# Kernel tuning notes

Hardware: AMD Instinct MI355X
Metric: run time of the kernel (lower is better)

## Reference

```python
import jax, jax.numpy as jnp
import numpy as np

# Static problem dims (match input_specs / init_kwargs)
B, NQ, C, H = 2, 900, 256, 8
HGT, WID = 64, 64            # single-scale feature map (input_spatial_shapes = [[64, 64]])
N = HGT * WID                # 4096 keys
DH = C // H                  # head dim 32
RPE_HID = 512
STRIDE = 16                  # feature_stride


def setup_inputs() -> dict:
    key = jax.random.key(0)
    ks = jax.random.split(key, 24)
    p = lambda k, shape: jax.random.normal(k, shape, jnp.float32) * 0.02
    # reference boxes (cx, cy, w, h) in pixel coords of a 1024x1024 image
    ref = jax.random.uniform(ks[0], (B, NQ, 1, 4), jnp.float32)
    ref = jnp.concatenate([ref[..., :2] * (WID * STRIDE), ref[..., 2:] * 128.0], axis=-1)
    return {
        "vggt_features": jnp.zeros((1,), jnp.float32),  # unused by forward (kept for signature fidelity)
        "query": jax.random.normal(ks[1], (B, NQ, C), jnp.float32),
        "reference_2d": ref,
        "k_input_flatten": jax.random.normal(ks[2], (B, N, C), jnp.float32),
        "v_input_flatten": jax.random.normal(ks[3], (B, N, C), jnp.float32),
        "input_spatial_shapes": jnp.array([[HGT, WID]], jnp.int32),
        "input_padding_mask": jnp.zeros((B, N), jnp.bool_),
        # cpb_mlp1 (x) and cpb_mlp2 (y): Linear(2,512)+ReLU+Linear(512,H,no bias); stored as [in,out]
        "W1x": p(ks[4], (2, RPE_HID)), "b1x": jnp.zeros((RPE_HID,), jnp.float32), "W2x": p(ks[5], (RPE_HID, H)),
        "W1y": p(ks[6], (2, RPE_HID)), "b1y": jnp.zeros((RPE_HID,), jnp.float32), "W2y": p(ks[7], (RPE_HID, H)),
        "Wq": p(ks[8], (C, C)), "bq": jnp.zeros((C,), jnp.float32),
        "Wk": p(ks[9], (C, C)), "bk": jnp.zeros((C,), jnp.float32),
        "Wv": p(ks[10], (C, C)), "bv": jnp.zeros((C,), jnp.float32),
        "Wp": p(ks[11], (C, C)), "bp": jnp.zeros((C,), jnp.float32),
    }


def _mlp(d, W1, b1, W2):
    return jax.nn.relu(d @ W1 + b1) @ W2


def reference(vggt_features, query, reference_2d, k_input_flatten, v_input_flatten,
              input_spatial_shapes, input_padding_mask,
              W1x, b1x, W2x, W1y, b1y, W2y, Wq, bq, Wk, bk, Wv, bv, Wp, bp):
    h, w = HGT, WID  # static (input_spatial_shapes[0] == [HGT, WID])
    scale = DH ** -0.5
    # cxcywh -> xyxy: [B, NQ, 1, 4]
    xyxy = jnp.concatenate([reference_2d[..., :2] - reference_2d[..., 2:] / 2,
                            reference_2d[..., :2] + reference_2d[..., 2:] / 2], axis=-1)
    # pixel-center grid coords (linspace(0.5, w-0.5, w) * stride)
    pos_x = ((jnp.arange(w, dtype=jnp.float32) + 0.5) * STRIDE)[None, None, :, None]
    pos_y = ((jnp.arange(h, dtype=jnp.float32) + 0.5) * STRIDE)[None, None, :, None]
    delta_x = xyxy[..., 0::2] - pos_x  # [B, NQ, w, 2]  (x1, x2 rel. to columns)
    delta_y = xyxy[..., 1::2] - pos_y  # [B, NQ, h, 2]  (y1, y2 rel. to rows)
    rpe_x = _mlp(delta_x, W1x, b1x, W2x)  # [B, NQ, w, H]
    rpe_y = _mlp(delta_y, W1y, b1y, W2y)  # [B, NQ, h, H]
    # broadcast add over (row, col) then flatten spatial -> [B, H, NQ, N]
    rpe = (rpe_x[:, :, None] + rpe_y[:, :, :, None]).reshape(B, NQ, h * w, H).transpose(0, 3, 1, 2)
    q = (query @ Wq + bq).reshape(B, NQ, H, DH).transpose(0, 2, 1, 3) * scale  # [B,H,NQ,DH]
    k = (k_input_flatten @ Wk + bk).reshape(B, N, H, DH).transpose(0, 2, 1, 3)  # [B,H,N,DH]
    v = (v_input_flatten @ Wv + bv).reshape(B, N, H, DH).transpose(0, 2, 1, 3)  # [B,H,N,DH]
    attn = jnp.einsum('bhqd,bhkd->bhqk', q, k) + rpe
    attn = attn + input_padding_mask[:, None, None, :].astype(attn.dtype) * (-100.0)
    # torch.clip_ to finfo(min,max) is an identity on finite values; softmax follows
    attn = jax.nn.softmax(attn, axis=-1)
    x = jnp.einsum('bhqk,bhkd->bhqd', attn, v).transpose(0, 2, 1, 3).reshape(B, NQ, C)
    return x @ Wp + bp
```

## Files before the change

kernel.cpp:

```cpp
#include <hip/hip_runtime.h>
#include <hip/hip_bf16.h>
#include <cmath>

#define B_ 2
#define NQ_ 900
#define N_ 4096
#define LOG2E 1.4426950408889634f

typedef __attribute__((ext_vector_type(4))) float f32x4;
typedef __attribute__((ext_vector_type(8))) short s16x8;
typedef __attribute__((ext_vector_type(8))) _Float16 f16x8;

__device__ inline short f2bf(float x) {
    union { __hip_bfloat16 b; short s; } u;
    u.b = __float2bfloat16(x);
    return u.s;
}
__device__ inline short f2h(float x) {
    _Float16 h = (_Float16)x;
    return __builtin_bit_cast(short, h);
}

template <int CTRL>
__device__ inline float dppf(float x) {
    int xi = __builtin_bit_cast(int, x);
    int r = __builtin_amdgcn_update_dpp(xi, xi, CTRL, 0xF, 0xF, true);
    return __builtin_bit_cast(float, r);
}
__device__ inline float rowmax16(float v) {
    v = fmaxf(v, dppf<0x121>(v));
    v = fmaxf(v, dppf<0x122>(v));
    v = fmaxf(v, dppf<0x124>(v));
    v = fmaxf(v, dppf<0x128>(v));
    return v;
}
__device__ inline float rowsum16(float v) {
    v += dppf<0x121>(v);
    v += dppf<0x122>(v);
    v += dppf<0x124>(v);
    v += dppf<0x128>(v);
    return v;
}

__global__ __launch_bounds__(256) void stage1_kernel(
    const float* __restrict__ query, const float* __restrict__ kin,
    const float* __restrict__ vin,
    const float* __restrict__ Wq, const float* __restrict__ Wk,
    const float* __restrict__ Wv, const float* __restrict__ Wp,
    const float* __restrict__ bqv, const float* __restrict__ bkv,
    const float* __restrict__ bvv,
    unsigned short* __restrict__ qbf, unsigned short* __restrict__ kbf,
    unsigned short* __restrict__ vbf, float qscale,
    const float* __restrict__ ref2d,
    const float* __restrict__ W1x, const float* __restrict__ b1x,
    const float* __restrict__ W1y, const float* __restrict__ b1y,
    const float* __restrict__ W2x, const float* __restrict__ W2y,
    float* __restrict__ rpe_x, float* __restrict__ rpe_y,
    unsigned short* __restrict__ wph, unsigned short* __restrict__ wpl)
{
    __shared__ uint4 smem[2560];
    const int bx = blockIdx.x;
    const int tid = threadIdx.x;
    const int w = tid >> 6, l = tid & 63, quad = l >> 4, l15 = l & 15;

    if (bx < 285) {
        short* Bb = (short*)smem;
        const int mtx = bx < 29 ? 0 : (bx < 157 ? 1 : 2);
        const int tile = bx - (mtx == 0 ? 0 : mtx == 1 ? 29 : 157);
        const int m0 = tile * 64;
        const float* X = mtx == 0 ? query : mtx == 1 ? kin : vin;
        const float* W = mtx == 0 ? Wq : mtx == 1 ? Wk : Wv;
        const float* bias = mtx == 0 ? bqv : mtx == 1 ? bkv : bvv;
        unsigned short* Y = mtx == 0 ? qbf : mtx == 1 ? kbf : vbf;
        const int M = mtx == 0 ? 1800 : 8192;
        const float alpha = mtx == 0 ? qscale : 1.0f;
        const int rows_per_b = mtx == 0 ? 900 : 4096;
        const int ROWS = mtx == 0 ? 960 : 4096;
        const int wq = tid & 3, mm = tid >> 2;

        s16x8 afr[8];
        {
            const int arow = m0 + w * 16 + l15;
            const bool avalid = arow < M;
            const float* xr = X + (size_t)arow * 256;
            #pragma unroll
            for (int kc = 0; kc < 8; ++kc) {
                float4 a0 = make_float4(0.f, 0.f, 0.f, 0.f), a1 = a0;
                if (avalid) {
                    a0 = *(const float4*)(xr + kc * 32 + quad * 8);
                    a1 = *(const float4*)(xr + kc * 32 + quad * 8 + 4);
                }
                unsigned pk0 = (unsigned)(unsigned short)f2bf(a0.x) | ((unsigned)(unsigned short)f2bf(a0.y) << 16);
                unsigned pk1 = (unsigned)(unsigned short)f2bf(a0.z) | ((unsigned)(unsigned short)f2bf(a0.w) << 16);
                unsigned pk2 = (unsigned)(unsigned short)f2bf(a1.x) | ((unsigned)(unsigned short)f2bf(a1.y) << 16);
                unsigned pk3 = (unsigned)(unsigned short)f2bf(a1.z) | ((unsigned)(unsigned short)f2bf(a1.w) << 16);
                uint4 pk = make_uint4(pk0, pk1, pk2, pk3);
                afr[kc] = __builtin_bit_cast(s16x8, pk);
            }
        }

        for (int nt0 = 0; nt0 < 4; ++nt0) {
            const int n0 = nt0 * 64;
            {
                const float* wcol = W + n0 + mm;
                #pragma unroll
                for (int it = 0; it < 8; ++it) {
                    int g2 = it * 4 + wq;
                    uint4 wk4;
                    wk4.x = (unsigned)(unsigned short)f2bf(wcol[(g2 * 8 + 0) * 256])
                          | ((unsigned)(unsigned short)f2bf(wcol[(g2 * 8 + 1) * 256]) << 16);
                    wk4.y = (unsigned)(unsigned short)f2bf(wcol[(g2 * 8 + 2) * 256])
                          | ((unsigned)(unsigned short)f2bf(wcol[(g2 * 8 + 3) * 256]) << 16);
                    wk4.z = (unsigned)(unsigned short)f2bf(wcol[(g2 * 8 + 4) * 256])
                          | ((unsigned)(unsigned short)f2bf(wcol[(g2 * 8 + 5) * 256]) << 16);
                    wk4.w = (unsigned)(unsigned short)f2bf(wcol[(g2 * 8 + 6) * 256])
                          | ((unsigned)(unsigned short)f2bf(wcol[(g2 * 8 + 7) * 256]) << 16);
                    *(uint4*)(Bb + (it * 256 + mm * 4 + wq) * 8) = wk4;
                }
            }
            __syncthreads();

            f32x4 acc[4] = {{0.f,0.f,0.f,0.f},{0.f,0.f,0.f,0.f},{0.f,0.f,0.f,0.f},{0.f,0.f,0.f,0.f}};
            #pragma unroll
            for (int kc = 0; kc < 8; ++kc) {
                #pragma unroll
                for (int nt = 0; nt < 4; ++nt) {
                    s16x8 bf = *(const s16x8*)(Bb + (kc * 256 + (nt * 16 + l15) * 4 + quad) * 8);
                    acc[nt] = __builtin_amdgcn_mfma_f32_16x16x32_bf16(afr[kc], bf, acc[nt], 0, 0, 0);
                }
            }

            #pragma unroll
            for (int nt = 0; nt < 4; ++nt) {
                int n = n0 + nt * 16 + l15;
                float bs = bias[n];
                int h = n >> 5, d = n & 31;
                #pragma unroll
                for (int r = 0; r < 4; ++r) {
                    int row = m0 + w * 16 + quad * 4 + r;
                    if (row < M) {
                        int b = row / rows_per_b;
                        int pos = row - b * rows_per_b;
                        Y[((size_t)(b * 8 + h) * ROWS + pos) * 32 + d] =
                            (unsigned short)f2bf((acc[nt][r] + bs) * alpha);
                    }
                }
            }
            __syncthreads();
        }
    } else if (bx < 735) {
        short* sw2h = (short*)smem;
        short* sw2l = (short*)smem + 8192;
        float4* sUV = (float4*)(smem + 2048);
        const int bq0 = (bx - 285) * 4;

        for (int i = tid; i < 8192; i += 256) {
            int g = i >> 3, j = i & 7;
            int kcg = g >> 6, rr = g & 63, n = rr >> 2, q4 = rr & 3;
            int k = kcg * 32 + q4 * 8 + j;
            float val = ((n < 8) ? W2x[k * 8 + n] : W2y[k * 8 + (n - 8)]) * LOG2E;
            _Float16 hi = (_Float16)val;
            sw2h[i] = __builtin_bit_cast(short, hi);
            sw2l[i] = f2h(val - (float)hi);
        }

        const int k0 = tid, k1 = tid + 256;
        const float w1x0a = W1x[k0], w1x1a = W1x[512 + k0];
        const float w1y0a = W1y[k0], w1y1a = W1y[512 + k0];
        const float bxa = b1x[k0], bya = b1y[k0];
        const float vxa = -(w1x0a + w1x1a), vya = -(w1y0a + w1y1a);
        const float w1x0b = W1x[k1], w1x1b = W1x[512 + k1];
        const float w1y0b = W1y[k1], w1y1b = W1y[512 + k1];
        const float bxb = b1x[k1], byb = b1y[k1];
        const float vxb = -(w1x0b + w1x1b), vyb = -(w1y0b + w1y1b);

        const int wrow = w;
        const int row = wrow * 16 + l15;
        const float pc = (row + 0.5f) * 16.0f;

        for (int qi = 0; qi < 4; ++qi) {
            const int bq = bq0 + qi;
            {
                const float4 bb = *(const float4*)(ref2d + (size_t)bq * 4);
                float x1 = bb.x - bb.z * 0.5f, x2 = bb.x + bb.z * 0.5f;
                float y1 = bb.y - bb.w * 0.5f, y2 = bb.y + bb.w * 0.5f;
                sUV[k0] = make_float4(fmaf(w1x0a, x1, fmaf(w1x1a, x2, bxa)), vxa,
                                      fmaf(w1y0a, y1, fmaf(w1y1a, y2, bya)), vya);
                sUV[k1] = make_float4(fmaf(w1x0b, x1, fmaf(w1x1b, x2, bxb)), vxb,
                                      fmaf(w1y0b, y1, fmaf(w1y1b, y2, byb)), vyb);
            }
            __syncthreads();

            f32x4 accx = {0.f, 0.f, 0.f, 0.f}, accy = {0.f, 0.f, 0.f, 0.f};
            for (int kc = 0; kc < 16; ++kc) {
                f16x8 axh, axl, ayh, ayl;
                #pragma unroll
                for (int i = 0; i < 8; ++i) {
                    float4 u = sUV[kc * 32 + quad * 8 + i];
                    float hx = fmaxf(fmaf(u.y, pc, u.x), 0.f);
                    float hy = fmaxf(fmaf(u.w, pc, u.z), 0.f);
                    _Float16 xh = (_Float16)hx;
                    _Float16 yh = (_Float16)hy;
                    axh[i] = xh;
                    axl[i] = (_Float16)(hx - (float)xh);
                    ayh[i] = yh;
                    ayl[i] = (_Float16)(hy - (float)yh);
                }
                f16x8 bh = *(const f16x8*)(sw2h + (kc * 64 + l15 * 4 + quad) * 8);
                f16x8 bl = *(const f16x8*)(sw2l + (kc * 64 + l15 * 4 + quad) * 8);
                accx = __builtin_amdgcn_mfma_f32_16x16x32_f16(axh, bh, accx, 0, 0, 0);
                accx = __builtin_amdgcn_mfma_f32_16x16x32_f16(axh, bl, accx, 0, 0, 0);
                accx = __builtin_amdgcn_mfma_f32_16x16x32_f16(axl, bh, accx, 0, 0, 0);
                accy = __builtin_amdgcn_mfma_f32_16x16x32_f16(ayh, bh, accy, 0, 0, 0);
                accy = __builtin_amdgcn_mfma_f32_16x16x32_f16(ayh, bl, accy, 0, 0, 0);
                accy = __builtin_amdgcn_mfma_f32_16x16x32_f16(ayl, bh, accy, 0, 0, 0);
            }

            #pragma unroll
            for (int rr = 0; rr < 4; ++rr) {
                int row_out = wrow * 16 + quad * 4 + rr;
                if (l15 < 8) rpe_x[((size_t)l15 * 1800 + bq) * 64 + row_out] = accx[rr];
                else         rpe_y[((size_t)(l15 - 8) * 1800 + bq) * 64 + row_out] = accy[rr];
            }
            __syncthreads();
        }
    } else {
        const int tile = bx - 735;
        const int kt = tile >> 2, ntile = tile & 3;
        unsigned short* th = (unsigned short*)smem;
        unsigned short* tl = th + 64 * 72;
        #pragma unroll
        for (int p = 0; p < 4; ++p) {
            int kl = p * 16 + (tid >> 4);
            int nl = (tid & 15) * 4;
            float4 v = *(const float4*)(Wp + (size_t)(kt * 64 + kl) * 256 + ntile * 64 + nl);
            float vv[4] = {v.x, v.y, v.z, v.w};
            #pragma unroll
            for (int i = 0; i < 4; ++i) {
                _Float16 h = (_Float16)vv[i];
                th[(nl + i) * 72 + kl] = (unsigned short)__builtin_bit_cast(short, h);
                tl[(nl + i) * 72 + kl] = (unsigned short)f2h(vv[i] - (float)h);
            }
        }
        __syncthreads();
        #pragma unroll
        for (int p = 0; p < 2; ++p) {
            int nl = p * 32 + (tid >> 3);
            int k8 = (tid & 7) * 8;
            uint4 pk;
            unsigned short* ps = (unsigned short*)&pk;
            #pragma unroll
            for (int j = 0; j < 8; ++j) ps[j] = th[nl * 72 + k8 + j];
            *(uint4*)(wph + (size_t)(ntile * 64 + nl) * 256 + kt * 64 + k8) = pk;
            #pragma unroll
            for (int j = 0; j < 8; ++j) ps[j] = tl[nl * 72 + k8 + j];
            *(uint4*)(wpl + (size_t)(ntile * 64 + nl) * 256 + kt * 64 + k8) = pk;
        }
    }
}

__global__ __launch_bounds__(256) void outproj_kernel(
    const float* __restrict__ X,
    const unsigned short* __restrict__ wph, const unsigned short* __restrict__ wpl,
    const float* __restrict__ bias, float* __restrict__ Y, int M)
{
    const int tid = threadIdx.x;
    const int m0 = blockIdx.x * 64, n0 = blockIdx.y * 64;
    const int w = tid >> 6, l = tid & 63, quad = l >> 4, l15 = l & 15;

    const int arow = m0 + w * 16 + l15;
    const bool avalid = arow < M;
    const float* xr = X + (size_t)arow * 256;

    f16x8 ah[8], al[8];
    #pragma unroll
    for (int kc = 0; kc < 8; ++kc) {
        float4 a0 = make_float4(0.f, 0.f, 0.f, 0.f), a1 = a0;
        if (avalid) {
            a0 = *(const float4*)(xr + kc * 32 + quad * 8);
            a1 = *(const float4*)(xr + kc * 32 + quad * 8 + 4);
        }
        float av[8] = {a0.x, a0.y, a0.z, a0.w, a1.x, a1.y, a1.z, a1.w};
        #pragma unroll
        for (int j = 0; j < 8; ++j) {
            _Float16 h = (_Float16)av[j];
            ah[kc][j] = h;
            al[kc][j] = (_Float16)(av[j] - (float)h);
        }
    }

    f32x4 acc[4] = {{0.f,0.f,0.f,0.f},{0.f,0.f,0.f,0.f},{0.f,0.f,0.f,0.f},{0.f,0.f,0.f,0.f}};
    #pragma unroll
    for (int kc = 0; kc < 8; ++kc) {
        #pragma unroll
        for (int nt = 0; nt < 4; ++nt) {
            size_t gb = (size_t)(n0 + nt * 16 + l15) * 256 + kc * 32 + quad * 8;
            f16x8 bh = *(const f16x8*)(wph + gb);
            f16x8 bl = *(const f16x8*)(wpl + gb);
            acc[nt] = __builtin_amdgcn_mfma_f32_16x16x32_f16(ah[kc], bh, acc[nt], 0, 0, 0);
            acc[nt] = __builtin_amdgcn_mfma_f32_16x16x32_f16(ah[kc], bl, acc[nt], 0, 0, 0);
            acc[nt] = __builtin_amdgcn_mfma_f32_16x16x32_f16(al[kc], bh, acc[nt], 0, 0, 0);
        }
    }

    #pragma unroll
    for (int nt = 0; nt < 4; ++nt) {
        int n = n0 + nt * 16 + l15;
        float bs = bias[n];
        #pragma unroll
        for (int r = 0; r < 4; ++r) {
            int row = m0 + w * 16 + quad * 4 + r;
            if (row < M)
                Y[(size_t)row * 256 + n] = acc[nt][r] + bs;
        }
    }
}

__global__ __launch_bounds__(512, 4) void attn_mfma_kernel(
    const unsigned short* __restrict__ qb16, const unsigned short* __restrict__ kb16,
    const unsigned short* __restrict__ vb16,
    const float* __restrict__ rpe_x, const float* __restrict__ rpe_y,
    const unsigned char* __restrict__ mask, float* __restrict__ xout)
{
    __shared__ short skf[4 * 2048];
    __shared__ short svt[4 * 2048];
    __shared__ short spb[8 * 544];
    __shared__ float ry[32 * 65];
    __shared__ unsigned long long smaskb[64];
    __shared__ float sm[8][16], sl[8][16], sLf[32];

    const int tid = threadIdx.x;
    const int qb = blockIdx.x, h = blockIdx.y, b = blockIdx.z;
    const int q0 = qb * 32;
    const int w = tid >> 6, l = tid & 63;
    const int qsub = w >> 2, g = w & 3;
    const int quad = l >> 4, l15 = l & 15;

    const unsigned short* qg = qb16 + (size_t)(b * 8 + h) * 960 * 32;
    const unsigned short* kg = kb16 + (size_t)(b * 8 + h) * 4096 * 32;
    const unsigned short* vg = vb16 + (size_t)(b * 8 + h) * 4096 * 32;
    const float* rxh = rpe_x + ((size_t)h * 1800 + b * NQ_) * 64;
    const float* ryh = rpe_y + ((size_t)h * 1800 + b * NQ_) * 64;

    for (int i = tid; i < 2048; i += 512) {
        int qq = q0 + (i >> 6), pos = i & 63;
        float vy = 0.f;
        if (qq < NQ_)
            vy = ryh[(size_t)qq * 64 + pos];
        ry[(i >> 6) * 65 + pos] = vy;
    }
    #pragma unroll
    for (int j = 0; j < 8; ++j) {
        int c = w * 8 + j;
        unsigned long long bits = __ballot(mask[(size_t)b * N_ + c * 64 + l] != 0);
        if (l == 0) smaskb[c] = bits;
    }

    s16x8 qa = *(const s16x8*)(qg + (size_t)(q0 + qsub * 16 + l15) * 32 + quad * 8);

    f32x4 rx4[4];
    #pragma unroll
    for (int t = 0; t < 4; ++t)
        #pragma unroll
        for (int r = 0; r < 4; ++r) {
            int qq = q0 + qsub * 16 + quad * 4 + r;
            rx4[t][r] = (qq < NQ_) ? rxh[(size_t)qq * 64 + t * 16 + l15] : 0.f;
        }

    const int sg = tid >> 7, role = (tid >> 6) & 1, stl = tid & 63;
    int eoff[4];
    if (role == 0) {
        #pragma unroll
        for (int t = 0; t < 4; ++t)
            eoff[t] = (t * 16 + (stl & 15)) * 32 + (stl >> 4) * 8;
    } else {
        #pragma unroll
        for (int t = 0; t < 4; ++t)
            eoff[t] = stl * 32 + t * 8;
    }
    const unsigned short* src = role ? vg : kg;

    uint4 pf[4];
    {
        size_t cb = (size_t)(sg * 16) * 2048;
        #pragma unroll
        for (int t = 0; t < 4; ++t) pf[t] = *(const uint4*)(src + cb + eoff[t]);
    }

    float mrow[4] = {-INFINITY, -INFINITY, -INFINITY, -INFINITY};
    float lrow[4] = {0.f, 0.f, 0.f, 0.f};
    f32x4 acc0 = {0.f, 0.f, 0.f, 0.f}, acc1 = {0.f, 0.f, 0.f, 0.f};
    short* pw = spb + w * 544;

    for (int i = 0; i < 16; ++i) {
        __syncthreads();
        if (role == 0) {
            #pragma unroll
            for (int t = 0; t < 4; ++t)
                *(uint4*)(skf + sg * 2048 + (t * 64 + stl) * 8) = pf[t];
        } else {
            short* vtw = svt + sg * 2048;
            #pragma unroll
            for (int t = 0; t < 4; ++t) {
                const unsigned short* pv = (const unsigned short*)&pf[t];
                #pragma unroll
                for (int j = 0; j < 8; ++j) {
                    int d = t * 8 + j;
                    vtw[d * 64 + (((stl >> 3) ^ (d & 7)) << 3) + (stl & 7)] = (short)pv[j];
                }
            }
        }
        __syncthreads();

        {
            int inext = (i + 1 < 16) ? i + 1 : 15;
            size_t cb = (size_t)(sg * 16 + inext) * 2048;
            #pragma unroll
            for (int t = 0; t < 4; ++t) pf[t] = *(const uint4*)(src + cb + eoff[t]);
        }

        const int cgc = g * 16 + i;
        const short* kf = skf + g * 2048;

        f32x4 sc[4];
        #pragma unroll
        for (int t = 0; t < 4; ++t) {
            s16x8 kb = *(const s16x8*)(kf + (t * 64 + l) * 8);
            sc[t] = __builtin_amdgcn_mfma_f32_16x16x32_bf16(qa, kb, rx4[t], 0, 0, 0);
        }
        float ryv[4];
        #pragma unroll
        for (int r = 0; r < 4; ++r)
            ryv[r] = ry[(qsub * 16 + quad * 4 + r) * 65 + cgc];
        unsigned long long mb = smaskb[cgc];
        if (mb) {
            #pragma unroll
            for (int t = 0; t < 4; ++t) {
                float mk = ((mb >> (t * 16 + l15)) & 1ULL) ? -144.2695f : 0.f;
                #pragma unroll
                for (int r = 0; r < 4; ++r) sc[t][r] += mk;
            }
        }

        float cmr[4];
        #pragma unroll
        for (int r = 0; r < 4; ++r)
            cmr[r] = fmaxf(fmaxf(sc[0][r], sc[1][r]), fmaxf(sc[2][r], sc[3][r])) + ryv[r];

        int ok = (cmr[0] <= mrow[0] + 8.f) & (cmr[1] <= mrow[1] + 8.f)
               & (cmr[2] <= mrow[2] + 8.f) & (cmr[3] <= mrow[3] + 8.f);
        if (!__all(ok)) {
            #pragma unroll
            for (int r = 0; r < 4; ++r) {
                float cm = rowmax16(cmr[r]);
                float mnew = fmaxf(mrow[r], cm);
                float al = exp2f(mrow[r] - mnew);
                mrow[r] = mnew;
                lrow[r] *= al;
                acc0[r] *= al;
                acc1[r] *= al;
            }
        }

        float msub[4];
        #pragma unroll
        for (int r = 0; r < 4; ++r) msub[r] = mrow[r] - ryv[r];
        #pragma unroll
        for (int t = 0; t < 4; ++t)
            #pragma unroll
            for (int r = 0; r < 4; ++r)
                sc[t][r] = exp2f(sc[t][r] - msub[r]);
        #pragma unroll
        for (int r = 0; r < 4; ++r)
            lrow[r] += (sc[0][r] + sc[1][r]) + (sc[2][r] + sc[3][r]);

        const short* vt = svt + g * 2048;
        #pragma unroll
        for (int hh = 0; hh < 2; ++hh) {
            #pragma unroll
            for (int tt = 0; tt < 2; ++tt) {
                int t = hh * 2 + tt;
                int gphys = (tt * 2 + (l15 >> 3)) ^ quad;
                #pragma unroll
                for (int r = 0; r < 4; ++r)
                    pw[(gphys * 17 + quad * 4 + r) * 8 + (l15 & 7)] = f2bf(sc[t][r]);
            }
            int gph_r = quad ^ (l15 >> 2);
            s16x8 pa  = *(const s16x8*)(pw + (gph_r * 17 + l15) * 8);
            int ksw = ((hh * 4 + quad) ^ (l15 & 7)) * 8;
            s16x8 vb0 = *(const s16x8*)(vt + l15 * 64 + ksw);
            s16x8 vb1 = *(const s16x8*)(vt + (16 + l15) * 64 + ksw);
            acc0 = __builtin_amdgcn_mfma_f32_16x16x32_bf16(pa, vb0, acc0, 0, 0, 0);
            acc1 = __builtin_amdgcn_mfma_f32_16x16x32_bf16(pa, vb1, acc1, 0, 0, 0);
        }
    }

    #pragma unroll
    for (int r = 0; r < 4; ++r) lrow[r] = rowsum16(lrow[r]);

    __syncthreads();
    if (l15 == 0) {
        #pragma unroll
        for (int r = 0; r < 4; ++r) {
            sm[w][quad * 4 + r] = mrow[r];
            sl[w][quad * 4 + r] = lrow[r];
        }
    }
    __syncthreads();
    float wgt[4], L4[4];
    #pragma unroll
    for (int r = 0; r < 4; ++r) {
        int qrow = quad * 4 + r;
        float mm = -INFINITY;
        #pragma unroll
        for (int gg = 0; gg < 4; ++gg) mm = fmaxf(mm, sm[qsub * 4 + gg][qrow]);
        float LL = 0.f;
        #pragma unroll
        for (int gg = 0; gg < 4; ++gg)
            LL += exp2f(sm[qsub * 4 + gg][qrow] - mm) * sl[qsub * 4 + gg][qrow];
        wgt[r] = exp2f(mrow[r] - mm);
        L4[r] = LL;
    }
    if (g == 0 && l15 == 0) {
        #pragma unroll
        for (int r = 0; r < 4; ++r) sLf[qsub * 16 + quad * 4 + r] = L4[r];
    }

    float* obuf = (float*)skf;
    for (int gg = 0; gg < 4; ++gg) {
        if (g == gg) {
            #pragma unroll
            for (int r = 0; r < 4; ++r) {
                int idx = (qsub * 16 + quad * 4 + r) * 33 + l15;
                float v0 = wgt[r] * acc0[r];
                float v1 = wgt[r] * acc1[r];
                if (gg == 0) { obuf[idx] = v0; obuf[idx + 16] = v1; }
                else         { obuf[idx] += v0; obuf[idx + 16] += v1; }
            }
        }
        __syncthreads();
    }

    for (int i = tid; i < 1024; i += 512) {
        int ql = i >> 5, d = i & 31;
        int qq = q0 + ql;
        if (qq < NQ_)
            xout[(size_t)(b * NQ_ + qq) * 256 + h * 32 + d] = obuf[ql * 33 + d] / sLf[ql];
    }
}

extern "C" void kernel_launch(void* const* d_in, const int* in_sizes, int n_in,
                              void* d_out, int out_size, void* d_ws, size_t ws_size,
                              hipStream_t stream)
{
    const float* query = (const float*)d_in[1];
    const float* ref2d = (const float*)d_in[2];
    const float* kin   = (const float*)d_in[3];
    const float* vin   = (const float*)d_in[4];
    const unsigned char* mask = (const unsigned char*)d_in[6];
    const float* W1x = (const float*)d_in[7];
    const float* b1x = (const float*)d_in[8];
    const float* W2x = (const float*)d_in[9];
    const float* W1y = (const float*)d_in[10];
    const float* b1y = (const float*)d_in[11];
    const float* W2y = (const float*)d_in[12];
    const float* Wq  = (const float*)d_in[13];
    const float* bq  = (const float*)d_in[14];
    const float* Wk  = (const float*)d_in[15];
    const float* bk  = (const float*)d_in[16];
    const float* Wv  = (const float*)d_in[17];
    const float* bv  = (const float*)d_in[18];
    const float* Wp  = (const float*)d_in[19];
    const float* bp  = (const float*)d_in[20];

    char* wsb = (char*)d_ws;
    unsigned short* qbf = (unsigned short*)(wsb);
    unsigned short* kbf = (unsigned short*)(wsb +   983040);
    unsigned short* vbf = (unsigned short*)(wsb +  5177344);
    float* rxws = (float*)(wsb +  9371648);
    float* ryws = (float*)(wsb + 13058048);
    float* xws  = (float*)(wsb + 16744448);
    unsigned short* wph = (unsigned short*)(wsb + 18587648);
    unsigned short* wpl = (unsigned short*)(wsb + 18718720);
    float* out  = (float*)d_out;

    const float qscale = LOG2E / sqrtf(32.0f);

    stage1_kernel<<<751, 256, 0, stream>>>(
        query, kin, vin, Wq, Wk, Wv, Wp, bq, bk, bv, qbf, kbf, vbf, qscale,
        ref2d, W1x, b1x, W1y, b1y, W2x, W2y, rxws, ryws, wph, wpl);
    attn_mfma_kernel<<<dim3(29, 8, B_), 512, 0, stream>>>(
        qbf, kbf, vbf, rxws, ryws, mask, xws);
    outproj_kernel<<<dim3(29, 4), 256, 0, stream>>>(
        xws, wph, wpl, bp, out, 1800);
}
```

Measured before the change: 200.4 us.

## Fuse output projection into attention kernel via last-arriving-block counter

```diff
diff --git a/kernel.cpp b/kernel.cpp
--- a/kernel.cpp
+++ b/kernel.cpp
@@ -56,7 +56,8 @@
     const float* __restrict__ W1y, const float* __restrict__ b1y,
     const float* __restrict__ W2x, const float* __restrict__ W2y,
     float* __restrict__ rpe_x, float* __restrict__ rpe_y,
-    unsigned short* __restrict__ wph, unsigned short* __restrict__ wpl)
+    unsigned short* __restrict__ wph, unsigned short* __restrict__ wpl,
+    unsigned int* __restrict__ cnt)
 {
     __shared__ uint4 smem[2560];
     const int bx = blockIdx.x;
@@ -227,6 +228,7 @@
     } else {
         const int tile = bx - 735;
         const int kt = tile >> 2, ntile = tile & 3;
+        if (tile == 0 && tid < 58) cnt[tid] = 0;
         unsigned short* th = (unsigned short*)smem;
         unsigned short* tl = th + 64 * 72;
         #pragma unroll
@@ -259,68 +261,14 @@
     }
 }
 
-__global__ __launch_bounds__(256) void outproj_kernel(
-    const float* __restrict__ X,
-    const unsigned short* __restrict__ wph, const unsigned short* __restrict__ wpl,
-    const float* __restrict__ bias, float* __restrict__ Y, int M)
-{
-    const int tid = threadIdx.x;
-    const int m0 = blockIdx.x * 64, n0 = blockIdx.y * 64;
-    const int w = tid >> 6, l = tid & 63, quad = l >> 4, l15 = l & 15;
-
-    const int arow = m0 + w * 16 + l15;
-    const bool avalid = arow < M;
-    const float* xr = X + (size_t)arow * 256;
-
-    f16x8 ah[8], al[8];
-    #pragma unroll
-    for (int kc = 0; kc < 8; ++kc) {
-        float4 a0 = make_float4(0.f, 0.f, 0.f, 0.f), a1 = a0;
-        if (avalid) {
-            a0 = *(const float4*)(xr + kc * 32 + quad * 8);
-            a1 = *(const float4*)(xr + kc * 32 + quad * 8 + 4);
-        }
-        float av[8] = {a0.x, a0.y, a0.z, a0.w, a1.x, a1.y, a1.z, a1.w};
-        #pragma unroll
-        for (int j = 0; j < 8; ++j) {
-            _Float16 h = (_Float16)av[j];
-            ah[kc][j] = h;
-            al[kc][j] = (_Float16)(av[j] - (float)h);
-        }
-    }
-
-    f32x4 acc[4] = {{0.f,0.f,0.f,0.f},{0.f,0.f,0.f,0.f},{0.f,0.f,0.f,0.f},{0.f,0.f,0.f,0.f}};
-    #pragma unroll
-    for (int kc = 0; kc < 8; ++kc) {
-        #pragma unroll
-        for (int nt = 0; nt < 4; ++nt) {
-            size_t gb = (size_t)(n0 + nt * 16 + l15) * 256 + kc * 32 + quad * 8;
-            f16x8 bh = *(const f16x8*)(wph + gb);
-            f16x8 bl = *(const f16x8*)(wpl + gb);
-            acc[nt] = __builtin_amdgcn_mfma_f32_16x16x32_f16(ah[kc], bh, acc[nt], 0, 0, 0);
-            acc[nt] = __builtin_amdgcn_mfma_f32_16x16x32_f16(ah[kc], bl, acc[nt], 0, 0, 0);
-            acc[nt] = __builtin_amdgcn_mfma_f32_16x16x32_f16(al[kc], bh, acc[nt], 0, 0, 0);
-        }
-    }
-
-    #pragma unroll
-    for (int nt = 0; nt < 4; ++nt) {
-        int n = n0 + nt * 16 + l15;
-        float bs = bias[n];
-        #pragma unroll
-        for (int r = 0; r < 4; ++r) {
-            int row = m0 + w * 16 + quad * 4 + r;
-            if (row < M)
-                Y[(size_t)row * 256 + n] = acc[nt][r] + bs;
-        }
-    }
-}
-
 __global__ __launch_bounds__(512, 4) void attn_mfma_kernel(
     const unsigned short* __restrict__ qb16, const unsigned short* __restrict__ kb16,
     const unsigned short* __restrict__ vb16,
     const float* __restrict__ rpe_x, const float* __restrict__ rpe_y,
-    const unsigned char* __restrict__ mask, float* __restrict__ xout)
+    const unsigned char* __restrict__ mask, float* __restrict__ xout,
+    const unsigned short* __restrict__ wph, const unsigned short* __restrict__ wpl,
+    const float* __restrict__ bp, float* __restrict__ out,
+    unsigned int* __restrict__ cnt)
 {
     __shared__ short skf[4 * 2048];
     __shared__ short svt[4 * 2048];
@@ -328,6 +276,7 @@
     __shared__ float ry[32 * 65];
     __shared__ unsigned long long smaskb[64];
     __shared__ float sm[8][16], sl[8][16], sLf[32];
+    __shared__ unsigned int sArrive;
 
     const int tid = threadIdx.x;
     const int qb = blockIdx.x, h = blockIdx.y, b = blockIdx.z;
@@ -546,6 +495,64 @@
         int qq = q0 + ql;
         if (qq < NQ_)
             xout[(size_t)(b * NQ_ + qq) * 256 + h * 32 + d] = obuf[ql * 33 + d] / sLf[ql];
+    }
+
+    __threadfence();
+    __syncthreads();
+    if (tid == 0)
+        sArrive = atomicAdd(&cnt[b * 29 + qb], 1u);
+    __syncthreads();
+    if (sArrive != 7u) return;
+    __threadfence();
+
+    {
+        const int rh = w & 1, cg = w >> 1;
+        const int qq = q0 + rh * 16 + l15;
+        const bool avalid = qq < NQ_;
+        const float* xr = xout + (size_t)(b * NQ_ + qq) * 256;
+
+        f16x8 ah[8], al[8];
+        #pragma unroll
+        for (int kc = 0; kc < 8; ++kc) {
+            float4 a0 = make_float4(0.f, 0.f, 0.f, 0.f), a1 = a0;
+            if (avalid) {
+                a0 = *(const float4*)(xr + kc * 32 + quad * 8);
+                a1 = *(const float4*)(xr + kc * 32 + quad * 8 + 4);
+            }
+            float av[8] = {a0.x, a0.y, a0.z, a0.w, a1.x, a1.y, a1.z, a1.w};
+            #pragma unroll
+            for (int j = 0; j < 8; ++j) {
+                _Float16 hh = (_Float16)av[j];
+                ah[kc][j] = hh;
+                al[kc][j] = (_Float16)(av[j] - (float)hh);
+            }
+        }
+
+        f32x4 acc[4] = {{0.f,0.f,0.f,0.f},{0.f,0.f,0.f,0.f},{0.f,0.f,0.f,0.f},{0.f,0.f,0.f,0.f}};
+        #pragma unroll
+        for (int kc = 0; kc < 8; ++kc) {
+            #pragma unroll
+            for (int nt = 0; nt < 4; ++nt) {
+                size_t gb = (size_t)(cg * 64 + nt * 16 + l15) * 256 + kc * 32 + quad * 8;
+                f16x8 bh = *(const f16x8*)(wph + gb);
+                f16x8 bl = *(const f16x8*)(wpl + gb);
+                acc[nt] = __builtin_amdgcn_mfma_f32_16x16x32_f16(ah[kc], bh, acc[nt], 0, 0, 0);
+                acc[nt] = __builtin_amdgcn_mfma_f32_16x16x32_f16(ah[kc], bl, acc[nt], 0, 0, 0);
+                acc[nt] = __builtin_amdgcn_mfma_f32_16x16x32_f16(al[kc], bh, acc[nt], 0, 0, 0);
+            }
+        }
+
+        #pragma unroll
+        for (int nt = 0; nt < 4; ++nt) {
+            int n = cg * 64 + nt * 16 + l15;
+            float bs = bp[n];
+            #pragma unroll
+            for (int r = 0; r < 4; ++r) {
+                int qrow = q0 + rh * 16 + quad * 4 + r;
+                if (qrow < NQ_)
+                    out[(size_t)(b * NQ_ + qrow) * 256 + n] = acc[nt][r] + bs;
+            }
+        }
     }
 }
 
@@ -582,15 +589,14 @@
     float* xws  = (float*)(wsb + 16744448);
     unsigned short* wph = (unsigned short*)(wsb + 18587648);
     unsigned short* wpl = (unsigned short*)(wsb + 18718720);
+    unsigned int* cnt   = (unsigned int*)(wsb + 18849792);
     float* out  = (float*)d_out;
 
     const float qscale = LOG2E / sqrtf(32.0f);
 
     stage1_kernel<<<751, 256, 0, stream>>>(
         query, kin, vin, Wq, Wk, Wv, Wp, bq, bk, bv, qbf, kbf, vbf, qscale,
-        ref2d, W1x, b1x, W1y, b1y, W2x, W2y, rxws, ryws, wph, wpl);
+        ref2d, W1x, b1x, W1y, b1y, W2x, W2y, rxws, ryws, wph, wpl, cnt);
     attn_mfma_kernel<<<dim3(29, 8, B_), 512, 0, stream>>>(
-        qbf, kbf, vbf, rxws, ryws, mask, xws);
-    outproj_kernel<<<dim3(29, 4), 256, 0, stream>>>(
-        xws, wph, wpl, bp, out, 1800);
-}
+        qbf, kbf, vbf, rxws, ryws, mask, xws, wph, wpl, bp, out, cnt);
+}
```

New measurement: 317.3 us. +58.3%, slower.
